# Kernel optimization log

Measured on AMD Instinct MI355X. Metric: run time of the kernel, lower is better.

## Reference

```python
import math
import jax, jax.numpy as jnp
import numpy as np

VOCAB = 50257
MAX_SEQ = 64
D_MODEL = 1024
N_HEADS = 16
N_LAYERS = 12
BATCH = 256
SEQ = 64


def setup_inputs() -> dict:
    key = jax.random.key(0)
    ks = jax.random.split(key, 16)
    s = 0.02
    d, L = D_MODEL, N_LAYERS
    inp = {
        "idx": jax.random.randint(ks[0], (BATCH, SEQ), 0, VOCAB, dtype=jnp.int32),
        "tok_emb": jax.random.normal(ks[1], (VOCAB, d), jnp.float32) * s,
        "pos_emb": jax.random.normal(ks[2], (MAX_SEQ, d), jnp.float32) * s,
        # per-block params stacked over layer dim [L, ...]; linear as x @ W + b
        "wqkv": jax.random.normal(ks[3], (L, d, 3 * d), jnp.float32) * s,
        "bqkv": jnp.zeros((L, 3 * d), jnp.float32),
        "wo": jax.random.normal(ks[4], (L, d, d), jnp.float32) * s,
        "bo": jnp.zeros((L, d), jnp.float32),
        "w1": jax.random.normal(ks[5], (L, d, 4 * d), jnp.float32) * s,
        "b1": jnp.zeros((L, 4 * d), jnp.float32),
        "w2": jax.random.normal(ks[6], (L, 4 * d, d), jnp.float32) * s,
        "b2": jnp.zeros((L, d), jnp.float32),
        "ln_g": jnp.ones((d,), jnp.float32),
        "ln_b": jnp.zeros((d,), jnp.float32),
        "out_w": jax.random.normal(ks[7], (d, d), jnp.float32) * s,
        "out_b": jnp.zeros((d,), jnp.float32),
    }
    return inp


def _attention(x, wqkv_l, bqkv_l, wo_l, bo_l):
    B, S, d = x.shape
    H = N_HEADS
    dh = d // H
    qkv = x @ wqkv_l + bqkv_l                      # [B,S,3d]
    q, k, v = jnp.split(qkv, 3, axis=-1)
    q = q.reshape(B, S, H, dh).transpose(0, 2, 1, 3)  # [B,H,S,dh]
    k = k.reshape(B, S, H, dh).transpose(0, 2, 1, 3)
    v = v.reshape(B, S, H, dh).transpose(0, 2, 1, 3)
    # NOTE: original scales by sqrt(d_model), not sqrt(head_dim)
    attn = jnp.einsum("bhqd,bhkd->bhqk", q, k) / math.sqrt(d)
    causal = jnp.tril(jnp.ones((S, S), bool))       # query i attends key j<=i
    attn = jnp.where(causal[None, None], attn, -jnp.inf)
    # NOTE: original applies softmax over dim=-2 (the QUERY axis)
    attn = jax.nn.softmax(attn, axis=-2)
    y = jnp.einsum("bhqk,bhkd->bhqd", attn, v)      # [B,H,S,dh]
    y = y.transpose(0, 2, 1, 3).reshape(B, S, d)
    return y @ wo_l + bo_l


def _layer_norm(x, g, b, eps=1e-5):
    mu = jnp.mean(x, axis=-1, keepdims=True)
    var = jnp.var(x, axis=-1, keepdims=True)
    return (x - mu) * jax.lax.rsqrt(var + eps) * g + b


def reference(idx, tok_emb, pos_emb, wqkv, bqkv, wo, bo, w1, b1, w2, b2,
              ln_g, ln_b, out_w, out_b):
    S = idx.shape[1]
    x = tok_emb[idx] + pos_emb[:S]                 # [B,S,d]
    for l in range(N_LAYERS):
        x = _attention(x, wqkv[l], bqkv[l], wo[l], bo[l]) + x
        h = jax.nn.gelu(x @ w1[l] + b1[l], approximate=False)
        x = h @ w2[l] + b2[l] + x
    x = _layer_norm(x, ln_g, ln_b)
    return x @ out_w + out_b
```

## Files before the change

kernel.cpp:

```cpp
#include <hip/hip_runtime.h>
#include <stdint.h>

typedef unsigned short u16;
typedef __bf16 bf16x8 __attribute__((ext_vector_type(8)));
typedef float f32x4 __attribute__((ext_vector_type(4)));

#define MT 16384

__device__ __forceinline__ u16 f2bf(float f) {
  union { float f; unsigned u; } x; x.f = f;
  unsigned r = x.u + 0x7fffu + ((x.u >> 16) & 1u);
  return (u16)(r >> 16);
}

#pragma clang diagnostic push
#pragma clang diagnostic ignored "-Waddress-space-conversion"
typedef __attribute__((address_space(1))) unsigned as1u;
typedef __attribute__((address_space(3))) unsigned as3u;
__device__ __forceinline__ void stage16(const u16* g, const u16* lbase) {
  __builtin_amdgcn_global_load_lds((as1u*)g, (as3u*)lbase, 16, 0, 0);
}
#pragma clang diagnostic pop

__global__ void __launch_bounds__(256)
transpose_cvt(const float* __restrict__ in, u16* __restrict__ out, int K, int N) {
  __shared__ float tile[32][33];
  const int k0 = blockIdx.y * 32, n0 = blockIdx.x * 32;
  const int tx = threadIdx.x, ty = threadIdx.y;
  #pragma unroll
  for (int r = 0; r < 32; r += 8)
    tile[ty + r][tx] = in[(size_t)(k0 + ty + r) * N + n0 + tx];
  __syncthreads();
  #pragma unroll
  for (int r = 0; r < 32; r += 8)
    out[(size_t)(n0 + ty + r) * K + k0 + tx] = f2bf(tile[tx][ty + r]);
}

__global__ void __launch_bounds__(256)
embed_kernel(const int* __restrict__ idx, const float* __restrict__ tok,
             const float* __restrict__ pos, float* __restrict__ x,
             u16* __restrict__ xb) {
  const int tk = blockIdx.x;
  const int s = tk & 63;
  const int id = idx[tk];
  const int t = threadIdx.x;
  float4 a = ((const float4*)(tok + (size_t)id * 1024))[t];
  float4 p = ((const float4*)(pos + (size_t)s * 1024))[t];
  float4 r; r.x = a.x + p.x; r.y = a.y + p.y; r.z = a.z + p.z; r.w = a.w + p.w;
  ((float4*)(x + (size_t)tk * 1024))[t] = r;
  u16* o = xb + (size_t)tk * 1024 + t * 4;
  o[0] = f2bf(r.x); o[1] = f2bf(r.y); o[2] = f2bf(r.z); o[3] = f2bf(r.w);
}

template<int EPI>
__global__ void __launch_bounds__(256, 3)
gemm128(const u16* __restrict__ A, const u16* __restrict__ Bt,
        const float* __restrict__ bias, float* __restrict__ resf,
        u16* __restrict__ outb, float* __restrict__ outf,
        int M, int N, int K, int gn) {
  __shared__ __align__(16) u16 lA[2][4096];
  __shared__ __align__(16) u16 lB[2][4096];
  const int t = threadIdx.x;
  const int lane = t & 63, w = t >> 6;
  const int wr = w >> 1, wc = w & 1;
  const int fr = lane & 15, fg = lane >> 4;

  const int nwg = gridDim.x;
  const int bid = blockIdx.x;
  const int s = (bid & 7) * (nwg >> 3) + (bid >> 3);
  const int tn = s % gn, tm = s / gn;
  const int m0 = tm * 128, n0 = tn * 128;

  const int rin = ((lane >> 3) << 1) + ((lane >> 2) & 1);
  const int fgl = (lane & 3) ^ ((lane >> 3) & 3);
  const u16* gA[2]; const u16* gB[2];
  #pragma unroll
  for (int i = 0; i < 2; ++i) {
    gA[i] = A  + (size_t)(m0 + (w * 2 + i) * 16 + rin) * K + fgl * 8;
    gB[i] = Bt + (size_t)(n0 + (w * 2 + i) * 16 + rin) * K + fgl * 8;
  }

  const int sub8 = ((fr & 1) * 4 + (fg ^ ((fr >> 1) & 3))) * 8;
  const int ar = wr * 2048 + (fr >> 1) * 64 + sub8;
  const int br = wc * 2048 + (fr >> 1) * 64 + sub8;

  f32x4 acc[4][4] = {};
  const int NT = K >> 5;

  #pragma unroll
  for (int i = 0; i < 2; ++i) {
    stage16(gA[i], &lA[0][(w * 2 + i) * 512]);
    stage16(gB[i], &lB[0][(w * 2 + i) * 512]);
  }
  __syncthreads();

  int cur = 0;
  for (int kt = 0; kt < NT; ++kt) {
    if (kt + 1 < NT) {
      const int ko = (kt + 1) << 5;
      #pragma unroll
      for (int i = 0; i < 2; ++i) {
        stage16(gA[i] + ko, &lA[cur ^ 1][(w * 2 + i) * 512]);
        stage16(gB[i] + ko, &lB[cur ^ 1][(w * 2 + i) * 512]);
      }
    }
    bf16x8 af[4], bv[4];
    #pragma unroll
    for (int m = 0; m < 4; ++m) af[m] = *(const bf16x8*)&lA[cur][ar + m * 512];
    #pragma unroll
    for (int n = 0; n < 4; ++n) bv[n] = *(const bf16x8*)&lB[cur][br + n * 512];
    #pragma unroll
    for (int m = 0; m < 4; ++m)
      #pragma unroll
      for (int n = 0; n < 4; ++n)
        acc[m][n] = __builtin_amdgcn_mfma_f32_16x16x32_bf16(af[m], bv[n], acc[m][n], 0, 0, 0);
    __syncthreads();
    cur ^= 1;
  }

  #pragma unroll
  for (int m = 0; m < 4; ++m) {
    const int row = m0 + wr * 64 + m * 16 + fg * 4;
    #pragma unroll
    for (int n = 0; n < 4; ++n) {
      const int col = n0 + wc * 64 + n * 16 + fr;
      const float bc = bias[col];
      #pragma unroll
      for (int i = 0; i < 4; ++i) {
        const size_t off = (size_t)(row + i) * N + col;
        float v = acc[m][n][i] + bc;
        if constexpr (EPI == 0) {
          outb[off] = f2bf(v);
        } else if constexpr (EPI == 1) {
          v = 0.5f * v * (1.0f + erff(v * 0.70710678118654752f));
          outb[off] = f2bf(v);
        } else if constexpr (EPI == 2) {
          v += resf[off];
          resf[off] = v;
          outb[off] = f2bf(v);
        } else {
          outf[off] = v;
        }
      }
    }
  }
}

__global__ void __launch_bounds__(256)
attn_kernel(const u16* __restrict__ qkv, u16* __restrict__ y) {
  __shared__ __align__(16) u16 qs[64][72];
  __shared__ __align__(16) u16 ks[64][72];
  __shared__ __align__(16) u16 vts[64][72];
  __shared__ __align__(16) float S[64][68];
  __shared__ float red[4][64];

  const int h = blockIdx.x, b = blockIdx.y;
  const int t = threadIdx.x;
  const int lane = t & 63, w = t >> 6;
  const int fr = lane & 15, fg = lane >> 4;

  #pragma unroll
  for (int it = 0; it < 2; ++it) {
    const int id = t + it * 256;
    const int row = id >> 3, seg = id & 7;
    const size_t gq = (size_t)(b * 64 + row) * 3072 + h * 64 + seg * 8;
    *(uint4*)&qs[row][seg * 8] = *(const uint4*)&qkv[gq];
    *(uint4*)&ks[row][seg * 8] = *(const uint4*)&qkv[gq + 1024];
  }
  {
    const int d = t & 63;
    #pragma unroll
    for (int it = 0; it < 16; ++it) {
      const int s = (t >> 6) + it * 4;
      vts[d][s] = qkv[(size_t)(b * 64 + s) * 3072 + 2048 + h * 64 + d];
    }
  }
  __syncthreads();

  f32x4 sa[4] = {};
  #pragma unroll
  for (int kk = 0; kk < 64; kk += 32) {
    bf16x8 qa = *(const bf16x8*)&qs[w * 16 + fr][kk + fg * 8];
    #pragma unroll
    for (int n = 0; n < 4; ++n) {
      bf16x8 kb = *(const bf16x8*)&ks[n * 16 + fr][kk + fg * 8];
      sa[n] = __builtin_amdgcn_mfma_f32_16x16x32_bf16(qa, kb, sa[n], 0, 0, 0);
    }
  }
  #pragma unroll
  for (int n = 0; n < 4; ++n)
    #pragma unroll
    for (int i = 0; i < 4; ++i) {
      const int row = w * 16 + fg * 4 + i, col = n * 16 + fr;
      S[row][col] = (row >= col) ? sa[n][i] * 0.03125f : -1e30f;
    }
  __syncthreads();

  const int c = t & 63, q4 = t >> 6;
  float mx = -1e30f;
  float e[16];
  #pragma unroll
  for (int i = 0; i < 16; ++i) mx = fmaxf(mx, S[q4 * 16 + i][c]);
  red[q4][c] = mx;
  __syncthreads();
  mx = fmaxf(fmaxf(red[0][c], red[1][c]), fmaxf(red[2][c], red[3][c]));
  float sum = 0.f;
  #pragma unroll
  for (int i = 0; i < 16; ++i) { e[i] = __expf(S[q4 * 16 + i][c] - mx); sum += e[i]; }
  __syncthreads();
  red[q4][c] = sum;
  __syncthreads();
  sum = red[0][c] + red[1][c] + red[2][c] + red[3][c];
  const float inv = 1.0f / sum;
  u16 (*P)[72] = qs;
  #pragma unroll
  for (int i = 0; i < 16; ++i)
    P[q4 * 16 + i][c] = f2bf(e[i] * inv);
  __syncthreads();

  f32x4 oa[4] = {};
  #pragma unroll
  for (int kk = 0; kk < 64; kk += 32) {
    bf16x8 pa = *(const bf16x8*)&P[w * 16 + fr][kk + fg * 8];
    #pragma unroll
    for (int n = 0; n < 4; ++n) {
      bf16x8 vb = *(const bf16x8*)&vts[n * 16 + fr][kk + fg * 8];
      oa[n] = __builtin_amdgcn_mfma_f32_16x16x32_bf16(pa, vb, oa[n], 0, 0, 0);
    }
  }
  #pragma unroll
  for (int n = 0; n < 4; ++n)
    #pragma unroll
    for (int i = 0; i < 4; ++i) {
      const int row = w * 16 + fg * 4 + i, col = n * 16 + fr;
      y[(size_t)(b * 64 + row) * 1024 + h * 64 + col] = f2bf(oa[n][i]);
    }
}

__global__ void __launch_bounds__(256)
ln_kernel(const float* __restrict__ x, const float* __restrict__ g,
          const float* __restrict__ bb, u16* __restrict__ xn) {
  __shared__ float sred[8];
  const int tok = blockIdx.x;
  const int t = threadIdx.x;
  const float4 v = ((const float4*)(x + (size_t)tok * 1024))[t];
  float s  = v.x + v.y + v.z + v.w;
  float ss = v.x * v.x + v.y * v.y + v.z * v.z + v.w * v.w;
  #pragma unroll
  for (int o = 32; o > 0; o >>= 1) {
    s  += __shfl_xor(s, o);
    ss += __shfl_xor(ss, o);
  }
  const int w = t >> 6;
  if ((t & 63) == 0) { sred[w] = s; sred[4 + w] = ss; }
  __syncthreads();
  s  = sred[0] + sred[1] + sred[2] + sred[3];
  ss = sred[4] + sred[5] + sred[6] + sred[7];
  const float mu = s * (1.0f / 1024.0f);
  const float var = ss * (1.0f / 1024.0f) - mu * mu;
  const float rs = rsqrtf(var + 1e-5f);
  const float4 gg = ((const float4*)g)[t];
  const float4 b4 = ((const float4*)bb)[t];
  u16* o = xn + (size_t)tok * 1024 + t * 4;
  o[0] = f2bf((v.x - mu) * rs * gg.x + b4.x);
  o[1] = f2bf((v.y - mu) * rs * gg.y + b4.y);
  o[2] = f2bf((v.z - mu) * rs * gg.z + b4.z);
  o[3] = f2bf((v.w - mu) * rs * gg.w + b4.w);
}

extern "C" void kernel_launch(void* const* d_in, const int* in_sizes, int n_in,
                              void* d_out, int out_size, void* d_ws, size_t ws_size,
                              hipStream_t stream) {
  const int*   idx     = (const int*)  d_in[0];
  const float* tok_emb = (const float*)d_in[1];
  const float* pos_emb = (const float*)d_in[2];
  const float* wqkv    = (const float*)d_in[3];
  const float* bqkv    = (const float*)d_in[4];
  const float* wo      = (const float*)d_in[5];
  const float* bo      = (const float*)d_in[6];
  const float* w1      = (const float*)d_in[7];
  const float* b1      = (const float*)d_in[8];
  const float* w2      = (const float*)d_in[9];
  const float* b2      = (const float*)d_in[10];
  const float* ln_g    = (const float*)d_in[11];
  const float* ln_b    = (const float*)d_in[12];
  const float* out_w   = (const float*)d_in[13];
  const float* out_b   = (const float*)d_in[14];

  char* p = (char*)d_ws;
  auto take = [&](size_t n) { char* r = p; p += (n + 255) & ~(size_t)255; return r; };
  u16*   wqkv_t = (u16*)  take((size_t)1024 * 3072 * 2);
  u16*   wo_t   = (u16*)  take((size_t)1024 * 1024 * 2);
  u16*   w1_t   = (u16*)  take((size_t)1024 * 4096 * 2);
  u16*   w2_t   = (u16*)  take((size_t)4096 * 1024 * 2);
  u16*   wout_t = (u16*)  take((size_t)1024 * 1024 * 2);
  float* xf     = (float*)take((size_t)MT * 1024 * 4);
  u16*   xb     = (u16*)  take((size_t)MT * 1024 * 2);
  u16*   yb     = (u16*)  take((size_t)MT * 1024 * 2);
  u16*   big    = (u16*)  take((size_t)MT * 4096 * 2);

  const dim3 tb(32, 8);
  embed_kernel<<<MT, 256, 0, stream>>>(idx, tok_emb, pos_emb, xf, xb);

  for (int l = 0; l < 12; ++l) {
    transpose_cvt<<<dim3(3072 / 32, 1024 / 32), tb, 0, stream>>>(
        wqkv + (size_t)l * 1024 * 3072, wqkv_t, 1024, 3072);
    transpose_cvt<<<dim3(1024 / 32, 1024 / 32), tb, 0, stream>>>(
        wo + (size_t)l * 1024 * 1024, wo_t, 1024, 1024);
    transpose_cvt<<<dim3(4096 / 32, 1024 / 32), tb, 0, stream>>>(
        w1 + (size_t)l * 1024 * 4096, w1_t, 1024, 4096);
    transpose_cvt<<<dim3(1024 / 32, 4096 / 32), tb, 0, stream>>>(
        w2 + (size_t)l * 4096 * 1024, w2_t, 4096, 1024);

    gemm128<0><<<(MT / 128) * (3072 / 128), 256, 0, stream>>>(
        xb, wqkv_t, bqkv + (size_t)l * 3072,
        nullptr, big, nullptr, MT, 3072, 1024, 3072 / 128);
    attn_kernel<<<dim3(16, 256), 256, 0, stream>>>(big, yb);
    gemm128<2><<<(MT / 128) * (1024 / 128), 256, 0, stream>>>(
        yb, wo_t, bo + (size_t)l * 1024,
        xf, xb, nullptr, MT, 1024, 1024, 1024 / 128);
    gemm128<1><<<(MT / 128) * (4096 / 128), 256, 0, stream>>>(
        xb, w1_t, b1 + (size_t)l * 4096,
        nullptr, big, nullptr, MT, 4096, 1024, 4096 / 128);
    gemm128<2><<<(MT / 128) * (1024 / 128), 256, 0, stream>>>(
        big, w2_t, b2 + (size_t)l * 1024,
        xf, xb, nullptr, MT, 1024, 4096, 1024 / 128);
  }

  transpose_cvt<<<dim3(1024 / 32, 1024 / 32), tb, 0, stream>>>(out_w, wout_t, 1024, 1024);
  ln_kernel<<<MT, 256, 0, stream>>>(xf, ln_g, ln_b, yb);
  gemm128<3><<<(MT / 128) * (1024 / 128), 256, 0, stream>>>(
      yb, wout_t, out_b, nullptr, nullptr, (float*)d_out, MT, 1024, 1024, 1024 / 128);
}
```

Before: 7.221 ms.

## Switch GEMMs to 256x128 tiles with 8 waves and asymmetric A/B prefetch

Replaces the 128x128, 256-thread GEMM with a 256x128, 512-thread kernel, so each B (weight) tile fetched from memory is reused across twice as many rows. The single-stage double buffer becomes a deeper pipeline: A is triple-buffered and prefetched two K-steps ahead, B is double-buffered one step ahead. Each step now has one raw barrier guarded by a manual vmcnt wait instead of two syncthreads. In exchange, the kernel uses more LDS (64 KB per block), which lowers occupancy. The wraparound indexing also issues redundant loads at the end of the K loop.

Result: slower. 7.401 ms (+2.5%).

```diff
diff --git a/kernel.cpp b/kernel.cpp
--- a/kernel.cpp
+++ b/kernel.cpp
@@ -53,12 +53,12 @@
 }
 
 template<int EPI>
-__global__ void __launch_bounds__(256, 3)
-gemm128(const u16* __restrict__ A, const u16* __restrict__ Bt,
-        const float* __restrict__ bias, float* __restrict__ resf,
-        u16* __restrict__ outb, float* __restrict__ outf,
-        int M, int N, int K, int gn) {
-  __shared__ __align__(16) u16 lA[2][4096];
+__global__ void __launch_bounds__(512, 4)
+gemm256x128(const u16* __restrict__ A, const u16* __restrict__ Bt,
+            const float* __restrict__ bias, float* __restrict__ resf,
+            u16* __restrict__ outb, float* __restrict__ outf,
+            int M, int N, int K, int gn) {
+  __shared__ __align__(16) u16 lA[3][8192];
   __shared__ __align__(16) u16 lB[2][4096];
   const int t = threadIdx.x;
   const int lane = t & 63, w = t >> 6;
@@ -69,16 +69,13 @@
   const int bid = blockIdx.x;
   const int s = (bid & 7) * (nwg >> 3) + (bid >> 3);
   const int tn = s % gn, tm = s / gn;
-  const int m0 = tm * 128, n0 = tn * 128;
+  const int m0 = tm * 256, n0 = tn * 128;
 
   const int rin = ((lane >> 3) << 1) + ((lane >> 2) & 1);
   const int fgl = (lane & 3) ^ ((lane >> 3) & 3);
-  const u16* gA[2]; const u16* gB[2];
-  #pragma unroll
-  for (int i = 0; i < 2; ++i) {
-    gA[i] = A  + (size_t)(m0 + (w * 2 + i) * 16 + rin) * K + fgl * 8;
-    gB[i] = Bt + (size_t)(n0 + (w * 2 + i) * 16 + rin) * K + fgl * 8;
-  }
+  const u16* gA0 = A  + (size_t)(m0 + (w * 2 + 0) * 16 + rin) * K + fgl * 8;
+  const u16* gA1 = A  + (size_t)(m0 + (w * 2 + 1) * 16 + rin) * K + fgl * 8;
+  const u16* gB  = Bt + (size_t)(n0 + w * 16 + rin) * K + fgl * 8;
 
   const int sub8 = ((fr & 1) * 4 + (fg ^ ((fr >> 1) & 3))) * 8;
   const int ar = wr * 2048 + (fr >> 1) * 64 + sub8;
@@ -87,36 +84,41 @@
   f32x4 acc[4][4] = {};
   const int NT = K >> 5;
 
-  #pragma unroll
-  for (int i = 0; i < 2; ++i) {
-    stage16(gA[i], &lA[0][(w * 2 + i) * 512]);
-    stage16(gB[i], &lB[0][(w * 2 + i) * 512]);
-  }
-  __syncthreads();
-
-  int cur = 0;
-  for (int kt = 0; kt < NT; ++kt) {
-    if (kt + 1 < NT) {
-      const int ko = (kt + 1) << 5;
-      #pragma unroll
-      for (int i = 0; i < 2; ++i) {
-        stage16(gA[i] + ko, &lA[cur ^ 1][(w * 2 + i) * 512]);
-        stage16(gB[i] + ko, &lB[cur ^ 1][(w * 2 + i) * 512]);
-      }
-    }
+  stage16(gB,        &lB[0][w * 512]);
+  stage16(gA0,       &lA[0][(w * 2 + 0) * 512]);
+  stage16(gA1,       &lA[0][(w * 2 + 1) * 512]);
+  stage16(gA0 + 32,  &lA[1][(w * 2 + 0) * 512]);
+  stage16(gA1 + 32,  &lA[1][(w * 2 + 1) * 512]);
+
+  int bufA = 0, bufB = 0;
+  for (int u = 0; u < NT; ++u) {
+    asm volatile("s_waitcnt vmcnt(2)" ::: "memory");
+    __builtin_amdgcn_s_barrier();
+    __builtin_amdgcn_sched_barrier(0);
+
+    int kt1 = u + 1; if (kt1 >= NT) kt1 -= NT;
+    int kt2 = u + 2; if (kt2 >= NT) kt2 -= NT;
+    const int ko1 = kt1 << 5, ko2 = kt2 << 5;
+    const int bA2 = (bufA + 2 >= 3) ? bufA - 1 : bufA + 2;
+    stage16(gB  + ko1, &lB[bufB ^ 1][w * 512]);
+    stage16(gA0 + ko2, &lA[bA2][(w * 2 + 0) * 512]);
+    stage16(gA1 + ko2, &lA[bA2][(w * 2 + 1) * 512]);
+
     bf16x8 af[4], bv[4];
     #pragma unroll
-    for (int m = 0; m < 4; ++m) af[m] = *(const bf16x8*)&lA[cur][ar + m * 512];
-    #pragma unroll
-    for (int n = 0; n < 4; ++n) bv[n] = *(const bf16x8*)&lB[cur][br + n * 512];
+    for (int m = 0; m < 4; ++m) af[m] = *(const bf16x8*)&lA[bufA][ar + m * 512];
+    #pragma unroll
+    for (int n = 0; n < 4; ++n) bv[n] = *(const bf16x8*)&lB[bufB][br + n * 512];
     #pragma unroll
     for (int m = 0; m < 4; ++m)
       #pragma unroll
       for (int n = 0; n < 4; ++n)
         acc[m][n] = __builtin_amdgcn_mfma_f32_16x16x32_bf16(af[m], bv[n], acc[m][n], 0, 0, 0);
-    __syncthreads();
-    cur ^= 1;
-  }
+
+    bufA = (bufA == 2) ? 0 : bufA + 1;
+    bufB ^= 1;
+  }
+  asm volatile("s_waitcnt vmcnt(0)" ::: "memory");
 
   #pragma unroll
   for (int m = 0; m < 4; ++m) {
@@ -312,23 +314,23 @@
     transpose_cvt<<<dim3(1024 / 32, 4096 / 32), tb, 0, stream>>>(
         w2 + (size_t)l * 4096 * 1024, w2_t, 4096, 1024);
 
-    gemm128<0><<<(MT / 128) * (3072 / 128), 256, 0, stream>>>(
+    gemm256x128<0><<<(MT / 256) * (3072 / 128), 512, 0, stream>>>(
         xb, wqkv_t, bqkv + (size_t)l * 3072,
         nullptr, big, nullptr, MT, 3072, 1024, 3072 / 128);
     attn_kernel<<<dim3(16, 256), 256, 0, stream>>>(big, yb);
-    gemm128<2><<<(MT / 128) * (1024 / 128), 256, 0, stream>>>(
+    gemm256x128<2><<<(MT / 256) * (1024 / 128), 512, 0, stream>>>(
         yb, wo_t, bo + (size_t)l * 1024,
         xf, xb, nullptr, MT, 1024, 1024, 1024 / 128);
-    gemm128<1><<<(MT / 128) * (4096 / 128), 256, 0, stream>>>(
+    gemm256x128<1><<<(MT / 256) * (4096 / 128), 512, 0, stream>>>(
         xb, w1_t, b1 + (size_t)l * 4096,
         nullptr, big, nullptr, MT, 4096, 1024, 4096 / 128);
-    gemm128<2><<<(MT / 128) * (1024 / 128), 256, 0, stream>>>(
+    gemm256x128<2><<<(MT / 256) * (1024 / 128), 512, 0, stream>>>(
         big, w2_t, b2 + (size_t)l * 1024,
         xf, xb, nullptr, MT, 1024, 4096, 1024 / 128);
   }
 
   transpose_cvt<<<dim3(1024 / 32, 1024 / 32), tb, 0, stream>>>(out_w, wout_t, 1024, 1024);
   ln_kernel<<<MT, 256, 0, stream>>>(xf, ln_g, ln_b, yb);
-  gemm128<3><<<(MT / 128) * (1024 / 128), 256, 0, stream>>>(
+  gemm256x128<3><<<(MT / 256) * (1024 / 128), 512, 0, stream>>>(
       yb, wout_t, out_b, nullptr, nullptr, (float*)d_out, MT, 1024, 1024, 1024 / 128);
 }
```
